# Optimization experiments

Measured on AMD Instinct MI355X. Metric: run time of the kernel, lower is better.

Reference implementation:

```python
import jax, jax.numpy as jnp
import numpy as np

EPS = 1e-12  # F.normalize eps


def _l2norm_c(x):
    # normalize over channel dim (axis=1), matching F.normalize(dim=1)
    n = jnp.sqrt(jnp.sum(x * x, axis=1, keepdims=True))
    return x / jnp.maximum(n, EPS)


def _rotate_all(q, angles_deg):
    """Rotate q [B,C,H,W] by every angle in angles_deg [A] via affine_grid +
    bilinear grid_sample (align_corners=False, zeros padding). Returns [A,B,C,H,W]."""
    B, C, H, W = q.shape
    th = jnp.deg2rad(angles_deg)
    # affine_grid align_corners=False output normalized coords
    xn = (2.0 * jnp.arange(W, dtype=q.dtype) + 1.0) / W - 1.0  # [W]
    yn = (2.0 * jnp.arange(H, dtype=q.dtype) + 1.0) / H - 1.0  # [H]
    c = jnp.cos(th)[:, None, None]
    s = jnp.sin(th)[:, None, None]
    gx = c * xn[None, None, :] - s * yn[None, :, None]  # [A,H,W]
    gy = s * xn[None, None, :] + c * yn[None, :, None]  # [A,H,W]
    # grid_sample align_corners=False: normalized -> input pixel coords
    ix = ((gx + 1.0) * W - 1.0) * 0.5
    iy = ((gy + 1.0) * H - 1.0) * 0.5
    x0 = jnp.floor(ix)
    y0 = jnp.floor(iy)
    wx = ix - x0  # frac weights
    wy = iy - y0
    x0i = x0.astype(jnp.int32)
    y0i = y0.astype(jnp.int32)

    def corner(yi, xi, w):
        valid = (xi >= 0) & (xi < W) & (yi >= 0) & (yi < H)  # zeros padding
        xc = jnp.clip(xi, 0, W - 1)
        yc = jnp.clip(yi, 0, H - 1)
        vals = q[:, :, yc, xc]  # advanced indexing -> [B,C,A,H,W]
        return vals * (w * valid.astype(q.dtype))[None, None]

    out = (corner(y0i, x0i, (1.0 - wx) * (1.0 - wy))
           + corner(y0i, x0i + 1, wx * (1.0 - wy))
           + corner(y0i + 1, x0i, (1.0 - wx) * wy)
           + corner(y0i + 1, x0i + 1, wx * wy))  # [B,C,A,H,W]
    return jnp.transpose(out, (2, 0, 1, 3, 4))  # [A,B,C,H,W]


def setup_inputs() -> dict:
    key = jax.random.key(0)
    ks = jax.random.split(key, 6)
    B, Cin, H, W, HID, A = 8, 768, 32, 32, 128, 36
    gallery_map = jax.random.normal(ks[0], (B, Cin, H, W), jnp.float32)
    query_map = jax.random.normal(ks[1], (B, Cin, H, W), jnp.float32)
    angles_deg = jnp.arange(A, dtype=jnp.float32) * 10.0 - 180.0
    Wg = jax.random.normal(ks[2], (HID, Cin), jnp.float32) / np.float32(np.sqrt(Cin))
    Wq = jax.random.normal(ks[3], (HID, Cin), jnp.float32) / np.float32(np.sqrt(Cin))
    W1 = jax.random.normal(ks[4], (HID, 4 * HID), jnp.float32) / np.float32(np.sqrt(4 * HID))
    b1 = jnp.zeros((HID,), jnp.float32)
    W2 = jax.random.normal(ks[5], (1, HID), jnp.float32) / np.float32(np.sqrt(HID))
    b2 = jnp.zeros((1,), jnp.float32)
    return {"gallery_map": gallery_map, "query_map": query_map, "Wg": Wg, "Wq": Wq,
            "W1": W1, "b1": b1, "W2": W2, "b2": b2, "angles_deg": angles_deg}


def reference(gallery_map, query_map, Wg, Wq, W1, b1, W2, b2, angles_deg):
    # 1x1-conv projections + channel L2 normalization (encode)
    g = _l2norm_c(jnp.einsum('oc,bchw->bohw', Wg, gallery_map))  # [B,HID,H,W]
    q = _l2norm_c(jnp.einsum('oc,bchw->bohw', Wq, query_map))    # [B,HID,H,W]
    qr = _rotate_all(q, angles_deg)  # [A,B,HID,H,W]
    HID = W1.shape[0]
    # head conv1 over cat([g, qr, g*qr, |g-qr|]) == sum of 4 block matmuls
    W1g, W1q, W1m, W1a = (W1[:, :HID], W1[:, HID:2 * HID],
                          W1[:, 2 * HID:3 * HID], W1[:, 3 * HID:])
    base = jnp.einsum('oc,bchw->bohw', W1g, g)  # angle-independent term
    h = (base[None]
         + jnp.einsum('oc,abchw->abohw', W1q, qr)
         + jnp.einsum('oc,abchw->abohw', W1m, g[None] * qr)
         + jnp.einsum('oc,abchw->abohw', W1a, jnp.abs(g[None] - qr))
         + b1[None, None, :, None, None])
    h = jax.nn.relu(h)  # [A,B,HID,H,W]
    H_, W_ = h.shape[-2], h.shape[-1]
    # head conv2 (HID->1) + spatial mean pool, per angle
    logits = jnp.einsum('c,abchw->ab', W2[0], h) / (H_ * W_) + b2[0]  # [A,B]
    return logits.T  # [B,A] matching torch.stack(logits, dim=1)
```

## Files before the change

kernel.cpp:

```cpp
#include <hip/hip_runtime.h>
#include <math.h>

#define B_   8
#define CIN  768
#define HID  128
#define NA   36
#define PP   1024

typedef _Float16 f16;
typedef __attribute__((ext_vector_type(2))) _Float16 f16x2;
typedef __attribute__((ext_vector_type(4))) _Float16 f16x4;
typedef __attribute__((ext_vector_type(8))) _Float16 f16x8;
typedef __attribute__((ext_vector_type(4))) float f32x4;

#define MFMA16(a, b, c) __builtin_amdgcn_mfma_f32_16x16x32_f16((a), (b), (c), 0, 0, 0)

__device__ inline f16x2 pkrtz(float a, float b) {
  union { __fp16 __attribute__((ext_vector_type(2))) r; f16x2 h; } u;
  u.r = __builtin_amdgcn_cvt_pkrtz(a, b);
  return u.h;
}

__device__ inline void rot_corners(float ct, float st, int y, int x,
                                   float w[4], int p[4]) {
  float xn = (2.0f * x + 1.0f) * (1.0f / 32.0f) - 1.0f;
  float yn = (2.0f * y + 1.0f) * (1.0f / 32.0f) - 1.0f;
  float gx = ct * xn - st * yn;
  float gy = st * xn + ct * yn;
  float ix = ((gx + 1.0f) * 32.0f - 1.0f) * 0.5f;
  float iy = ((gy + 1.0f) * 32.0f - 1.0f) * 0.5f;
  float x0f = floorf(ix), y0f = floorf(iy);
  float wx = ix - x0f, wy = iy - y0f;
  int x0 = (int)x0f, y0 = (int)y0f;
  int x1 = x0 + 1, y1 = y0 + 1;
  float vx0 = (x0 >= 0 && x0 < 32) ? 1.0f : 0.0f;
  float vx1 = (x1 >= 0 && x1 < 32) ? 1.0f : 0.0f;
  float vy0 = (y0 >= 0 && y0 < 32) ? 1.0f : 0.0f;
  float vy1 = (y1 >= 0 && y1 < 32) ? 1.0f : 0.0f;
  int cx0 = min(max(x0, 0), 31), cx1 = min(max(x1, 0), 31);
  int cy0 = min(max(y0, 0), 31), cy1 = min(max(y1, 0), 31);
  w[0] = (1.0f - wx) * (1.0f - wy) * vx0 * vy0;  p[0] = (cy0 << 5) + cx0;
  w[1] = wx * (1.0f - wy) * vx1 * vy0;           p[1] = (cy0 << 5) + cx1;
  w[2] = (1.0f - wx) * wy * vx0 * vy1;           p[2] = (cy1 << 5) + cx0;
  w[3] = wx * wy * vx1 * vy1;                    p[3] = (cy1 << 5) + cx1;
}

__global__ __launch_bounds__(256) void prep_k(
    const float* __restrict__ Wg, const float* __restrict__ Wq,
    const float* __restrict__ W1, const float* __restrict__ b2,
    f16* __restrict__ Wg_h, f16* __restrict__ Wq_h,
    f16* __restrict__ W1_h, float* __restrict__ out) {
  int idx = blockIdx.x * 256 + threadIdx.x;
  if (idx < B_ * NA) out[idx] = b2[0];
  if (idx < 32768) {
    int e = idx * 8;
    const float* src; f16* dst; int off;
    if (e < 98304)       { src = Wg; dst = Wg_h; off = e; }
    else if (e < 196608) { src = Wq; dst = Wq_h; off = e - 98304; }
    else                 { src = W1; dst = W1_h; off = e - 196608; }
    float4 lo = *(const float4*)(src + off);
    float4 hi = *(const float4*)(src + off + 4);
    f16x8 h;
    h[0] = (f16)lo.x; h[1] = (f16)lo.y; h[2] = (f16)lo.z; h[3] = (f16)lo.w;
    h[4] = (f16)hi.x; h[5] = (f16)hi.y; h[6] = (f16)hi.z; h[7] = (f16)hi.w;
    *(f16x8*)(dst + off) = h;
  }
}

#define WCH_S 264
#define PS_S  132
#define GN_S  136
__global__ __launch_bounds__(512, 4) void projfused_k(
    const float* __restrict__ gal, const float* __restrict__ qry,
    const f16* __restrict__ Wg_h, const f16* __restrict__ Wq_h,
    const f16* __restrict__ W1_h, const float* __restrict__ b1,
    f16* __restrict__ gout, f16* __restrict__ qout,
    float* __restrict__ baseb1) {
  __shared__ __align__(16) char LDSU[67584];
  f16*   Wch = (f16*)LDSU;
  float* ps  = (float*)LDSU;
  f16*   Gn  = (f16*)LDSU;
  f16*   W1l = (f16*)(LDSU + 8704);

  int pblk = blockIdx.x, b = blockIdx.y, z = blockIdx.z;
  const float* imgB = (z ? qry : gal) + (size_t)b * CIN * PP;
  const f16* Wm = z ? Wq_h : Wg_h;
  f16* dst = z ? qout : gout;
  int tid = threadIdx.x, lane = tid & 63, wv = tid >> 6;
  int q = lane >> 4, lr = lane & 15;
  int kw = wv & 3, mw = wv >> 2;
  int pw = pblk * 32 + mw * 16;

  f32x4 acc[8];
  #pragma unroll
  for (int t = 0; t < 8; t++) acc[t] = (f32x4){0.f, 0.f, 0.f, 0.f};

  int so = tid >> 2, sseg = (tid & 3) * 64;
  for (int cc = 0; cc < CIN; cc += 256) {
    #pragma unroll
    for (int j = 0; j < 8; j++)
      *(f16x8*)&Wch[so * WCH_S + sseg + j * 8] =
          *(const f16x8*)(Wm + so * CIN + cc + sseg + j * 8);
    __syncthreads();
    #pragma unroll
    for (int ks = 0; ks < 2; ks++) {
      int k0 = kw * 64 + ks * 32;
      const float* ip = imgB + (size_t)(cc + k0 + q * 8) * PP + pw + lr;
      float v0 = ip[0], v1 = ip[PP], v2 = ip[2 * PP], v3 = ip[3 * PP];
      float v4 = ip[4 * PP], v5 = ip[5 * PP], v6 = ip[6 * PP], v7 = ip[7 * PP];
      union { f16x8 v; f16x2 h[4]; } bf;
      bf.h[0] = pkrtz(v0, v1); bf.h[1] = pkrtz(v2, v3);
      bf.h[2] = pkrtz(v4, v5); bf.h[3] = pkrtz(v6, v7);
      #pragma unroll
      for (int og = 0; og < 8; og++) {
        f16x8 af = *(const f16x8*)&Wch[(og * 16 + lr) * WCH_S + k0 + q * 8];
        acc[og] = MFMA16(af, bf.v, acc[og]);
      }
    }
    __syncthreads();
  }

  #pragma unroll
  for (int og = 0; og < 8; og++)
    *(f32x4*)&ps[kw * (32 * PS_S) + (mw * 16 + lr) * PS_S + og * 16 + q * 4] = acc[og];
  __syncthreads();
  int pos = tid >> 4, oo = (tid & 15) * 8;
  f32x4 v0s = (f32x4){0.f,0.f,0.f,0.f}, v1s = (f32x4){0.f,0.f,0.f,0.f};
  #pragma unroll
  for (int k = 0; k < 4; k++) {
    v0s += *(const f32x4*)&ps[k * (32 * PS_S) + pos * PS_S + oo];
    v1s += *(const f32x4*)&ps[k * (32 * PS_S) + pos * PS_S + oo + 4];
  }
  float ss = v0s.x*v0s.x + v0s.y*v0s.y + v0s.z*v0s.z + v0s.w*v0s.w
           + v1s.x*v1s.x + v1s.y*v1s.y + v1s.z*v1s.z + v1s.w*v1s.w;
  ss += __shfl_xor(ss, 1); ss += __shfl_xor(ss, 2);
  ss += __shfl_xor(ss, 4); ss += __shfl_xor(ss, 8);
  float inv = 1.0f / fmaxf(sqrtf(ss), 1e-12f);
  f16x8 gn8;
  gn8[0] = (f16)(v0s.x*inv); gn8[1] = (f16)(v0s.y*inv);
  gn8[2] = (f16)(v0s.z*inv); gn8[3] = (f16)(v0s.w*inv);
  gn8[4] = (f16)(v1s.x*inv); gn8[5] = (f16)(v1s.y*inv);
  gn8[6] = (f16)(v1s.z*inv); gn8[7] = (f16)(v1s.w*inv);
  *(f16x8*)(dst + (size_t)((b << 10) + pblk * 32 + pos) * HID + oo) = gn8;

  if (z == 0) {
    __syncthreads();
    *(f16x8*)&Gn[pos * GN_S + oo] = gn8;
    {
      int o = tid >> 2, seg = (tid & 3) * 32;
      #pragma unroll
      for (int j = 0; j < 4; j++)
        *(f16x8*)&W1l[o * GN_S + seg + j * 8] =
            *(const f16x8*)(W1_h + o * 512 + seg + j * 8);
    }
    __syncthreads();
    int nw = wv & 3, mw2 = wv >> 2;
    f32x4 acc2[2];
    acc2[0] = (f32x4){0.f,0.f,0.f,0.f}; acc2[1] = (f32x4){0.f,0.f,0.f,0.f};
    #pragma unroll
    for (int ks = 0; ks < 4; ks++) {
      f16x8 bfv = *(const f16x8*)&Gn[(mw2 * 16 + lr) * GN_S + ks * 32 + q * 8];
      #pragma unroll
      for (int og2 = 0; og2 < 2; og2++) {
        f16x8 af = *(const f16x8*)&W1l[(nw * 32 + og2 * 16 + lr) * GN_S + ks * 32 + q * 8];
        acc2[og2] = MFMA16(af, bfv, acc2[og2]);
      }
    }
    #pragma unroll
    for (int og2 = 0; og2 < 2; og2++) {
      int o0 = nw * 32 + og2 * 16 + q * 4;
      float4 bb = *(const float4*)(b1 + o0);
      float4 r;
      r.x = acc2[og2][0] + bb.x; r.y = acc2[og2][1] + bb.y;
      r.z = acc2[og2][2] + bb.z; r.w = acc2[og2][3] + bb.w;
      *(float4*)(baseb1 + (size_t)((b << 10) + pblk * 32 + mw2 * 16 + lr) * HID + o0) = r;
    }
  }
}

__global__ __launch_bounds__(256, 3) void main_k(
    const f16* __restrict__ g_h, const f16* __restrict__ q_h,
    const float* __restrict__ baseb1, const f16* __restrict__ W1_h,
    const float* __restrict__ W2, const float* __restrict__ angles,
    float* __restrict__ out) {
  __shared__ f16 Xs[2][32 * 392];
  __shared__ float redl[24];
  int y = blockIdx.x, b = blockIdx.y;
  int tid = threadIdx.x;
  int lane = tid & 63, wv = tid >> 6;
  int q = lane >> 4, lr = lane & 15;
  int nq = wv * 32;

  f16x8 bfr[12][2];
  #pragma unroll
  for (int s = 0; s < 12; s++)
    #pragma unroll
    for (int ni = 0; ni < 2; ni++) {
      int o = nq + ni * 16 + lr;
      bfr[s][ni] = *(const f16x8*)(W1_h + o * 512 + 128 + s * 32 + q * 8);
    }

  float bacc[2][2][4];
  float w2v[2];
  #pragma unroll
  for (int ni = 0; ni < 2; ni++) w2v[ni] = W2[nq + ni * 16 + lr];
  #pragma unroll
  for (int mi = 0; mi < 2; mi++)
    #pragma unroll
    for (int r = 0; r < 4; r++) {
      int m = mi * 16 + q * 4 + r;
      #pragma unroll
      for (int ni = 0; ni < 2; ni++)
        bacc[mi][ni][r] = baseb1[(size_t)((b << 10) + (y << 5) + m) * HID + nq + ni * 16 + lr];
    }

  int bx = tid >> 3, ks = tid & 7;
  const f16* qB = q_h + (size_t)(b << 10) * HID;
  const f16* gB = g_h + (size_t)((b << 10) + (y << 5) + bx) * HID;

  float spart[6];

  for (int it = 0; it < 6; it++) {
    int a = blockIdx.z * 6 + it;
    float th = angles[a] * 0.017453292519943295f;
    float ct = cosf(th), st = sinf(th);
    f16* Xb = &Xs[it & 1][0];

    {
      float w4[4]; int p4[4];
      rot_corners(ct, st, y, bx, w4, p4);
      f16x2 wc[4];
      #pragma unroll
      for (int k = 0; k < 4; k++) {
        f16 h = (f16)w4[k];
        wc[k] = (f16x2){h, h};
      }
      const f16* c0p = qB + p4[0] * HID;
      const f16* c1p = qB + p4[1] * HID;
      const f16* c2p = qB + p4[2] * HID;
      const f16* c3p = qB + p4[3] * HID;
      #pragma unroll
      for (int cg = 0; cg < 2; cg++) {
        int c = ks * 16 + cg * 8;
        union U8 { f16x8 v; f16x2 h[4]; } u0, u1, u2, u3, gg, oq, om, oa;
        u0.v = *(const f16x8*)(c0p + c);
        u1.v = *(const f16x8*)(c1p + c);
        u2.v = *(const f16x8*)(c2p + c);
        u3.v = *(const f16x8*)(c3p + c);
        gg.v = *(const f16x8*)(gB + c);
        #pragma unroll
        for (int i = 0; i < 4; i++) {
          f16x2 qr = u0.h[i] * wc[0] + u1.h[i] * wc[1]
                   + u2.h[i] * wc[2] + u3.h[i] * wc[3];
          f16x2 mm = gg.h[i] * qr;
          union { f16x2 h; unsigned int u; } dd;
          dd.h = gg.h[i] - qr;
          dd.u &= 0x7fff7fffu;
          oq.h[i] = qr; om.h[i] = mm; oa.h[i] = dd.h;
        }
        *(f16x8*)&Xb[bx * 392 + c] = oq.v;
        *(f16x8*)&Xb[bx * 392 + 128 + c] = om.v;
        *(f16x8*)&Xb[bx * 392 + 256 + c] = oa.v;
      }
    }
    __syncthreads();

    f32x4 acc[2][2];
    #pragma unroll
    for (int i = 0; i < 2; i++)
      #pragma unroll
      for (int j = 0; j < 2; j++) acc[i][j] = (f32x4){0.f, 0.f, 0.f, 0.f};
    #pragma unroll
    for (int s = 0; s < 12; s++) {
      f16x8 a0 = *(const f16x8*)&Xb[(lr) * 392 + s * 32 + q * 8];
      f16x8 a1 = *(const f16x8*)&Xb[(16 + lr) * 392 + s * 32 + q * 8];
      acc[0][0] = MFMA16(a0, bfr[s][0], acc[0][0]);
      acc[0][1] = MFMA16(a0, bfr[s][1], acc[0][1]);
      acc[1][0] = MFMA16(a1, bfr[s][0], acc[1][0]);
      acc[1][1] = MFMA16(a1, bfr[s][1], acc[1][1]);
    }

    float s = 0.f;
    #pragma unroll
    for (int mi = 0; mi < 2; mi++)
      #pragma unroll
      for (int ni = 0; ni < 2; ni++)
        #pragma unroll
        for (int r = 0; r < 4; r++)
          s = fmaf(w2v[ni], fmaxf(acc[mi][ni][r] + bacc[mi][ni][r], 0.f), s);
    spart[it] = s;
  }

  #pragma unroll
  for (int it = 0; it < 6; it++) {
    float v = spart[it];
    #pragma unroll
    for (int off = 32; off > 0; off >>= 1) v += __shfl_down(v, off, 64);
    if (lane == 0) redl[wv * 6 + it] = v;
  }
  __syncthreads();
  if (tid < 6) {
    float tot = redl[tid] + redl[6 + tid] + redl[12 + tid] + redl[18 + tid];
    atomicAdd(&out[b * NA + blockIdx.z * 6 + tid], tot * (1.0f / 1024.0f));
  }
}

extern "C" void kernel_launch(void* const* d_in, const int* in_sizes, int n_in,
                              void* d_out, int out_size, void* d_ws, size_t ws_size,
                              hipStream_t stream) {
  const float* gal = (const float*)d_in[0];
  const float* qry = (const float*)d_in[1];
  const float* Wg  = (const float*)d_in[2];
  const float* Wq  = (const float*)d_in[3];
  const float* W1  = (const float*)d_in[4];
  const float* b1  = (const float*)d_in[5];
  const float* W2  = (const float*)d_in[6];
  const float* b2  = (const float*)d_in[7];
  const float* ang = (const float*)d_in[8];
  float* out = (float*)d_out;
  char* ws = (char*)d_ws;
  f16*   g_h    = (f16*)ws;
  f16*   q_h    = (f16*)(ws + (2u << 20));
  float* baseb1 = (float*)(ws + (4u << 20));
  f16*   Wg_h   = (f16*)(ws + (8u << 20));
  f16*   Wq_h   = (f16*)(ws + (8u << 20) + 196608);
  f16*   W1_h   = (f16*)(ws + (8u << 20) + 393216);

  hipLaunchKernelGGL(prep_k, dim3(128), dim3(256), 0, stream,
                     Wg, Wq, W1, b2, Wg_h, Wq_h, W1_h, out);
  hipLaunchKernelGGL(projfused_k, dim3(32, 8, 2), dim3(512), 0, stream,
                     gal, qry, Wg_h, Wq_h, W1_h, b1, g_h, q_h, baseb1);
  hipLaunchKernelGGL(main_k, dim3(32, 8, 6), dim3(256), 0, stream,
                     g_h, q_h, baseb1, W1_h, W2, ang, out);
}
```

Before: 167.6 us.

## Prefetch gather corners and image chunks; precompute rotation tables; seed accumulators with bias

In the projection kernel, the fp32 image values for the next 256-channel chunk are loaded into registers while the current chunk is computed, and the weight chunk is staged through registers before its LDS write. In the main kernel, the bilinear corner weights and indices for all six angles are computed once into shared-memory tables. The four corner gathers for the next angle are prefetched into a double-buffered register set, and the MFMA accumulators start from the base+bias values, so the separate add is gone. The goal is to hide global-load latency behind MFMA work, at the cost of higher register pressure, which is why launch bounds drop from 3 to 2 blocks per CU.

```diff
diff --git a/kernel.cpp b/kernel.cpp
--- a/kernel.cpp
+++ b/kernel.cpp
@@ -96,21 +96,37 @@
   for (int t = 0; t < 8; t++) acc[t] = (f32x4){0.f, 0.f, 0.f, 0.f};
 
   int so = tid >> 2, sseg = (tid & 3) * 64;
-  for (int cc = 0; cc < CIN; cc += 256) {
+  const float* ipb = imgB + (size_t)(kw * 64 + q * 8) * PP + pw + lr;
+
+  float fim[2][16];
+  #pragma unroll
+  for (int t = 0; t < 16; t++)
+    fim[0][t] = ipb[(size_t)((t >> 3) * 32 + (t & 7)) * PP];
+
+  #pragma unroll
+  for (int c3 = 0; c3 < 3; c3++) {
+    int cc = c3 << 8;
+    f16x8 w8[8];
     #pragma unroll
     for (int j = 0; j < 8; j++)
-      *(f16x8*)&Wch[so * WCH_S + sseg + j * 8] =
-          *(const f16x8*)(Wm + so * CIN + cc + sseg + j * 8);
-    __syncthreads();
-    #pragma unroll
-    for (int ks = 0; ks < 2; ks++) {
-      int k0 = kw * 64 + ks * 32;
-      const float* ip = imgB + (size_t)(cc + k0 + q * 8) * PP + pw + lr;
-      float v0 = ip[0], v1 = ip[PP], v2 = ip[2 * PP], v3 = ip[3 * PP];
-      float v4 = ip[4 * PP], v5 = ip[5 * PP], v6 = ip[6 * PP], v7 = ip[7 * PP];
+      w8[j] = *(const f16x8*)(Wm + so * CIN + cc + sseg + j * 8);
+    if (c3 < 2) {
+      #pragma unroll
+      for (int t = 0; t < 16; t++)
+        fim[(c3 + 1) & 1][t] =
+            ipb[(size_t)(((c3 + 1) << 8) + (t >> 3) * 32 + (t & 7)) * PP];
+    }
+    #pragma unroll
+    for (int j = 0; j < 8; j++)
+      *(f16x8*)&Wch[so * WCH_S + sseg + j * 8] = w8[j];
+    __syncthreads();
+    #pragma unroll
+    for (int ksi = 0; ksi < 2; ksi++) {
       union { f16x8 v; f16x2 h[4]; } bf;
-      bf.h[0] = pkrtz(v0, v1); bf.h[1] = pkrtz(v2, v3);
-      bf.h[2] = pkrtz(v4, v5); bf.h[3] = pkrtz(v6, v7);
+      const float* fp = &fim[c3 & 1][ksi * 8];
+      bf.h[0] = pkrtz(fp[0], fp[1]); bf.h[1] = pkrtz(fp[2], fp[3]);
+      bf.h[2] = pkrtz(fp[4], fp[5]); bf.h[3] = pkrtz(fp[6], fp[7]);
+      int k0 = kw * 64 + ksi * 32;
       #pragma unroll
       for (int og = 0; og < 8; og++) {
         f16x8 af = *(const f16x8*)&Wch[(og * 16 + lr) * WCH_S + k0 + q * 8];
@@ -158,11 +174,11 @@
     f32x4 acc2[2];
     acc2[0] = (f32x4){0.f,0.f,0.f,0.f}; acc2[1] = (f32x4){0.f,0.f,0.f,0.f};
     #pragma unroll
-    for (int ks = 0; ks < 4; ks++) {
-      f16x8 bfv = *(const f16x8*)&Gn[(mw2 * 16 + lr) * GN_S + ks * 32 + q * 8];
+    for (int ksj = 0; ksj < 4; ksj++) {
+      f16x8 bfv = *(const f16x8*)&Gn[(mw2 * 16 + lr) * GN_S + ksj * 32 + q * 8];
       #pragma unroll
       for (int og2 = 0; og2 < 2; og2++) {
-        f16x8 af = *(const f16x8*)&W1l[(nw * 32 + og2 * 16 + lr) * GN_S + ks * 32 + q * 8];
+        f16x8 af = *(const f16x8*)&W1l[(nw * 32 + og2 * 16 + lr) * GN_S + ksj * 32 + q * 8];
         acc2[og2] = MFMA16(af, bfv, acc2[og2]);
       }
     }
@@ -178,12 +194,14 @@
   }
 }
 
-__global__ __launch_bounds__(256, 3) void main_k(
+__global__ __launch_bounds__(256, 2) void main_k(
     const f16* __restrict__ g_h, const f16* __restrict__ q_h,
     const float* __restrict__ baseb1, const f16* __restrict__ W1_h,
     const float* __restrict__ W2, const float* __restrict__ angles,
     float* __restrict__ out) {
   __shared__ f16 Xs[2][32 * 392];
+  __shared__ float wtab[6][32][4];
+  __shared__ int   ptab[6][32][4];
   __shared__ float redl[24];
   int y = blockIdx.x, b = blockIdx.y;
   int tid = threadIdx.x;
@@ -191,6 +209,16 @@
   int q = lane >> 4, lr = lane & 15;
   int nq = wv * 32;
 
+  if (tid < 192) {
+    int it = tid >> 5, pos = tid & 31;
+    float th = angles[blockIdx.z * 6 + it] * 0.017453292519943295f;
+    float ct = cosf(th), st = sinf(th);
+    float w4[4]; int p4[4];
+    rot_corners(ct, st, y, pos, w4, p4);
+    *(float4*)&wtab[it][pos][0] = make_float4(w4[0], w4[1], w4[2], w4[3]);
+    *(int4*)&ptab[it][pos][0]   = make_int4(p4[0], p4[1], p4[2], p4[3]);
+  }
+
   f16x8 bfr[12][2];
   #pragma unroll
   for (int s = 0; s < 12; s++)
@@ -200,62 +228,69 @@
       bfr[s][ni] = *(const f16x8*)(W1_h + o * 512 + 128 + s * 32 + q * 8);
     }
 
-  float bacc[2][2][4];
   float w2v[2];
   #pragma unroll
   for (int ni = 0; ni < 2; ni++) w2v[ni] = W2[nq + ni * 16 + lr];
+
+  f32x4 binit[2][2];
   #pragma unroll
   for (int mi = 0; mi < 2; mi++)
     #pragma unroll
-    for (int r = 0; r < 4; r++) {
-      int m = mi * 16 + q * 4 + r;
-      #pragma unroll
-      for (int ni = 0; ni < 2; ni++)
-        bacc[mi][ni][r] = baseb1[(size_t)((b << 10) + (y << 5) + m) * HID + nq + ni * 16 + lr];
-    }
+    for (int ni = 0; ni < 2; ni++)
+      #pragma unroll
+      for (int r = 0; r < 4; r++) {
+        int m = mi * 16 + q * 4 + r;
+        binit[mi][ni][r] =
+            baseb1[(size_t)((b << 10) + (y << 5) + m) * HID + nq + ni * 16 + lr];
+      }
 
   int bx = tid >> 3, ks = tid & 7;
-  const f16* qB = q_h + (size_t)(b << 10) * HID;
-  const f16* gB = g_h + (size_t)((b << 10) + (y << 5) + bx) * HID;
+  const f16* qB = q_h + ((size_t)(b << 10)) * HID + ks * 16;
+  const f16* gB = g_h + (size_t)((b << 10) + (y << 5) + bx) * HID + ks * 16;
+  f16x8 gg[2] = { *(const f16x8*)gB, *(const f16x8*)(gB + 8) };
+
+  __syncthreads();
+
+  f16x8 u[2][2][4];
+  float4 wcur, wnxt;
+  {
+    wcur = *(const float4*)&wtab[0][bx][0];
+    int4 pt = *(const int4*)&ptab[0][bx][0];
+    #pragma unroll
+    for (int cg = 0; cg < 2; cg++) {
+      u[0][cg][0] = *(const f16x8*)(qB + pt.x * HID + cg * 8);
+      u[0][cg][1] = *(const f16x8*)(qB + pt.y * HID + cg * 8);
+      u[0][cg][2] = *(const f16x8*)(qB + pt.z * HID + cg * 8);
+      u[0][cg][3] = *(const f16x8*)(qB + pt.w * HID + cg * 8);
+    }
+  }
 
   float spart[6];
-
+  #pragma unroll
   for (int it = 0; it < 6; it++) {
-    int a = blockIdx.z * 6 + it;
-    float th = angles[a] * 0.017453292519943295f;
-    float ct = cosf(th), st = sinf(th);
-    f16* Xb = &Xs[it & 1][0];
-
+    int cur = it & 1;
+    f16* Xb = &Xs[cur][0];
     {
-      float w4[4]; int p4[4];
-      rot_corners(ct, st, y, bx, w4, p4);
       f16x2 wc[4];
-      #pragma unroll
-      for (int k = 0; k < 4; k++) {
-        f16 h = (f16)w4[k];
-        wc[k] = (f16x2){h, h};
-      }
-      const f16* c0p = qB + p4[0] * HID;
-      const f16* c1p = qB + p4[1] * HID;
-      const f16* c2p = qB + p4[2] * HID;
-      const f16* c3p = qB + p4[3] * HID;
+      wc[0] = (f16x2){(f16)wcur.x, (f16)wcur.x};
+      wc[1] = (f16x2){(f16)wcur.y, (f16)wcur.y};
+      wc[2] = (f16x2){(f16)wcur.z, (f16)wcur.z};
+      wc[3] = (f16x2){(f16)wcur.w, (f16)wcur.w};
       #pragma unroll
       for (int cg = 0; cg < 2; cg++) {
         int c = ks * 16 + cg * 8;
-        union U8 { f16x8 v; f16x2 h[4]; } u0, u1, u2, u3, gg, oq, om, oa;
-        u0.v = *(const f16x8*)(c0p + c);
-        u1.v = *(const f16x8*)(c1p + c);
-        u2.v = *(const f16x8*)(c2p + c);
-        u3.v = *(const f16x8*)(c3p + c);
-        gg.v = *(const f16x8*)(gB + c);
+        union U8 { f16x8 v; f16x2 h[4]; } u0, u1, u2, u3, gv, oq, om, oa;
+        u0.v = u[cur][cg][0]; u1.v = u[cur][cg][1];
+        u2.v = u[cur][cg][2]; u3.v = u[cur][cg][3];
+        gv.v = gg[cg];
         #pragma unroll
         for (int i = 0; i < 4; i++) {
           f16x2 qr = u0.h[i] * wc[0] + u1.h[i] * wc[1]
                    + u2.h[i] * wc[2] + u3.h[i] * wc[3];
-          f16x2 mm = gg.h[i] * qr;
-          union { f16x2 h; unsigned int u; } dd;
-          dd.h = gg.h[i] - qr;
-          dd.u &= 0x7fff7fffu;
+          f16x2 mm = gv.h[i] * qr;
+          union { f16x2 h; unsigned int uu; } dd;
+          dd.h = gv.h[i] - qr;
+          dd.uu &= 0x7fff7fffu;
           oq.h[i] = qr; om.h[i] = mm; oa.h[i] = dd.h;
         }
         *(f16x8*)&Xb[bx * 392 + c] = oq.v;
@@ -263,32 +298,41 @@
         *(f16x8*)&Xb[bx * 392 + 256 + c] = oa.v;
       }
     }
-    __syncthreads();
-
-    f32x4 acc[2][2];
-    #pragma unroll
-    for (int i = 0; i < 2; i++)
-      #pragma unroll
-      for (int j = 0; j < 2; j++) acc[i][j] = (f32x4){0.f, 0.f, 0.f, 0.f};
+    if (it < 5) {
+      wnxt = *(const float4*)&wtab[it + 1][bx][0];
+      int4 pt = *(const int4*)&ptab[it + 1][bx][0];
+      #pragma unroll
+      for (int cg = 0; cg < 2; cg++) {
+        u[cur ^ 1][cg][0] = *(const f16x8*)(qB + pt.x * HID + cg * 8);
+        u[cur ^ 1][cg][1] = *(const f16x8*)(qB + pt.y * HID + cg * 8);
+        u[cur ^ 1][cg][2] = *(const f16x8*)(qB + pt.z * HID + cg * 8);
+        u[cur ^ 1][cg][3] = *(const f16x8*)(qB + pt.w * HID + cg * 8);
+      }
+    }
+    __syncthreads();
+
+    f32x4 a00 = binit[0][0], a01 = binit[0][1];
+    f32x4 a10 = binit[1][0], a11 = binit[1][1];
     #pragma unroll
     for (int s = 0; s < 12; s++) {
-      f16x8 a0 = *(const f16x8*)&Xb[(lr) * 392 + s * 32 + q * 8];
-      f16x8 a1 = *(const f16x8*)&Xb[(16 + lr) * 392 + s * 32 + q * 8];
-      acc[0][0] = MFMA16(a0, bfr[s][0], acc[0][0]);
-      acc[0][1] = MFMA16(a0, bfr[s][1], acc[0][1]);
-      acc[1][0] = MFMA16(a1, bfr[s][0], acc[1][0]);
-      acc[1][1] = MFMA16(a1, bfr[s][1], acc[1][1]);
-    }
-
-    float s = 0.f;
-    #pragma unroll
-    for (int mi = 0; mi < 2; mi++)
-      #pragma unroll
-      for (int ni = 0; ni < 2; ni++)
-        #pragma unroll
-        for (int r = 0; r < 4; r++)
-          s = fmaf(w2v[ni], fmaxf(acc[mi][ni][r] + bacc[mi][ni][r], 0.f), s);
-    spart[it] = s;
+      f16x8 af0 = *(const f16x8*)&Xb[(lr) * 392 + s * 32 + q * 8];
+      f16x8 af1 = *(const f16x8*)&Xb[(16 + lr) * 392 + s * 32 + q * 8];
+      a00 = MFMA16(af0, bfr[s][0], a00);
+      a01 = MFMA16(af0, bfr[s][1], a01);
+      a10 = MFMA16(af1, bfr[s][0], a10);
+      a11 = MFMA16(af1, bfr[s][1], a11);
+    }
+
+    float sv = 0.f;
+    #pragma unroll
+    for (int r = 0; r < 4; r++) {
+      sv = fmaf(w2v[0], fmaxf(a00[r], 0.f), sv);
+      sv = fmaf(w2v[1], fmaxf(a01[r], 0.f), sv);
+      sv = fmaf(w2v[0], fmaxf(a10[r], 0.f), sv);
+      sv = fmaf(w2v[1], fmaxf(a11[r], 0.f), sv);
+    }
+    spart[it] = sv;
+    wcur = wnxt;
   }
 
   #pragma unroll
```

Measured after the change: 163.1 us. 2.7% less time.
